# Kernel tuning notes

Measured on AMD Instinct MI355X. Metric: run time of the kernel, lower is better.

## Reference

```python
import jax, jax.numpy as jnp
import numpy as np

B, T, E, H = 4, 2048, 1024, 16
HS = E // H  # head_size = 64


def setup_inputs() -> dict:
    key = jax.random.key(0)
    ks = jax.random.split(key, 5)
    x = jax.random.normal(ks[0], (B, T, E), jnp.float32)
    scale = 0.02
    Wq = jax.random.normal(ks[1], (H, E, HS), jnp.float32) * scale
    Wk = jax.random.normal(ks[2], (H, E, HS), jnp.float32) * scale
    Wv = jax.random.normal(ks[3], (H, E, HS), jnp.float32) * scale
    Wo = jax.random.normal(ks[4], (E, E), jnp.float32) * scale
    bo = jnp.zeros((E,), jnp.float32)
    return {"x": x, "Wq": Wq, "Wk": Wk, "Wv": Wv, "Wo": Wo, "bo": bo}


def reference(x, Wq, Wk, Wv, Wo, bo):
    b, t, e = x.shape
    # per-head projections, batched over heads
    Q = jnp.einsum('bte,hed->bhtd', x, Wq)  # (B,H,T,HS)
    K = jnp.einsum('bte,hed->bhtd', x, Wk)
    V = jnp.einsum('bte,hed->bhtd', x, Wv)
    # faithful quirk 1: scale by sqrt(embd_size), not sqrt(head_size)
    scores = jnp.einsum('bhtd,bhsd->bhts', Q, K) / jnp.sqrt(jnp.float32(e))
    mask = jnp.tril(jnp.ones((t, t), dtype=bool))  # (T_q, T_k)
    scores = jnp.where(mask[None, None, :, :], scores, -jnp.inf)
    # faithful quirk 2: original softmaxes over dim=1 of (B,Tq,Tk) = the QUERY axis
    attn = jax.nn.softmax(scores, axis=2)
    out = jnp.einsum('bhts,bhsd->bhtd', attn, V)  # (B,H,T,HS)
    out = out.transpose(0, 2, 1, 3).reshape(b, t, e)  # concat heads -> (B,T,E)
    return out @ Wo + bo
```

## Files before the change

### kernel.cpp

```cpp
#include <hip/hip_runtime.h>
#include <stdint.h>

#define Bn 4
#define Tn 2048
#define En 1024
#define Hn 16
#define HSn 64
#define BHn (Bn*Hn)
#define NRn (Bn*Tn)

#define CEXP 0.0450840831f

typedef __attribute__((ext_vector_type(8))) short short8;
typedef __attribute__((ext_vector_type(4))) float f32x4;
typedef __attribute__((ext_vector_type(16))) float f32x16;
typedef __attribute__((ext_vector_type(4))) unsigned int uint4w;

__device__ __forceinline__ unsigned short f2b(float f){
  union { float f; unsigned int u; } c; c.f = f;
  unsigned int u = c.u + 0x7FFFu + ((c.u >> 16) & 1u);
  return (unsigned short)(u >> 16);
}
__device__ __forceinline__ float b2f(unsigned short s){
  union { unsigned int u; float f; } c; c.u = ((unsigned int)s) << 16;
  return c.f;
}
__device__ __forceinline__ unsigned int cvtpk(float lo, float hi){
  unsigned int r;
  asm("v_cvt_pk_bf16_f32 %0, %1, %2" : "=v"(r) : "v"(lo), "v"(hi));
  return r;
}
__device__ __forceinline__ f32x4 mfma16(short8 a, short8 b, f32x4 c){
  return __builtin_amdgcn_mfma_f32_16x16x32_bf16(a, b, c, 0, 0, 0);
}
__device__ __forceinline__ f32x16 mfma32(short8 a, short8 b, f32x16 c){
  return __builtin_amdgcn_mfma_f32_32x32x16_bf16(a, b, c, 0, 0, 0);
}
__device__ __forceinline__ void gl16(const void* g, void* s){
  __builtin_amdgcn_global_load_lds((const __attribute__((address_space(1))) unsigned int*)g,
                                   (__attribute__((address_space(3))) unsigned int*)s, 16, 0, 0);
}
#define FENCE()    asm volatile("" ::: "memory")
#define WAITV(N)   asm volatile("s_waitcnt vmcnt(" #N ")" ::: "memory")
#define SBAR()     __builtin_amdgcn_s_barrier()

__global__ void k_cvt_x(const float* __restrict__ x, unsigned short* __restrict__ xb){
  int i = (blockIdx.x * blockDim.x + threadIdx.x) * 8;
  float4 a = *(const float4*)(x + i);
  float4 b = *(const float4*)(x + i + 4);
  alignas(16) unsigned short o[8] = {f2b(a.x),f2b(a.y),f2b(a.z),f2b(a.w),
                                     f2b(b.x),f2b(b.y),f2b(b.z),f2b(b.w)};
  *(uint4w*)(xb + i) = *(const uint4w*)o;
}

__global__ void k_wT(const float* __restrict__ Wq, const float* __restrict__ Wk,
                     const float* __restrict__ Wv, const float* __restrict__ Wo,
                     unsigned short* __restrict__ Wt, unsigned short* __restrict__ Wot)
{
  __shared__ unsigned short Ls[64*80];
  const int tid = threadIdx.x;
  const int ey = blockIdx.x, jt = blockIdx.y;
  const int e0 = ey*64;
  const float* src; int R, c0; unsigned short* outp;
  if (jt < 48){
    int sel = jt >> 4, h = jt & 15;
    const float* W = (sel==0)?Wq:((sel==1)?Wk:Wv);
    src = W + h*(En*HSn); R = HSn; c0 = 0;
    outp = Wt + jt*64*En;
  } else {
    src = Wo; R = En; c0 = (jt-48)*64;
    outp = Wot + (jt-48)*64*En;
  }
  {
    const int e = tid >> 2, cq = (tid & 3)*16;
    const float* p = src + (e0 + e)*R + c0 + cq;
    float vv[16];
    *(float4*)&vv[0]  = *(const float4*)(p);
    *(float4*)&vv[4]  = *(const float4*)(p+4);
    *(float4*)&vv[8]  = *(const float4*)(p+8);
    *(float4*)&vv[12] = *(const float4*)(p+12);
#pragma unroll
    for (int i = 0; i < 16; i++) Ls[(cq+i)*80 + e] = f2b(vv[i]);
  }
  __syncthreads();
  {
    const int c8 = tid & 7, r = tid >> 3;
#pragma unroll
    for (int rr0 = 0; rr0 < 2; rr0++){
      int rr = r + rr0*32;
      *(uint4w*)(outp + rr*En + e0 + c8*8) = *(const uint4w*)&Ls[rr*80 + c8*8];
    }
  }
}

__global__ void __launch_bounds__(256, 2)
k_qkv(const unsigned short* __restrict__ xb,
      const unsigned short* __restrict__ Wt,
      unsigned short* __restrict__ Qb, unsigned short* __restrict__ Kb,
      unsigned short* __restrict__ Vt)
{
  __shared__ unsigned short As[2][128*64];
  __shared__ unsigned short Bs[2][128*64];
  const int tid = threadIdx.x, lane = tid & 63, w = tid >> 6;
  const int wr = w >> 1, wc = w & 1;
  const int mb = blockIdx.x, nb = blockIdx.y;
  const int n0 = nb*128;
  const int sel = n0 >> 10;
  const int nj0 = n0 & 1023;
  const int l15 = lane & 15, kc = lane >> 4;
  const int r8 = lane >> 3, c7 = lane & 7;

  const unsigned short* xbase = xb + (mb*128)*En;
  const unsigned short* wbase = Wt + n0*En;

  f32x4 acc[4][4];
#pragma unroll
  for (int i = 0; i < 4; i++)
#pragma unroll
    for (int j = 0; j < 4; j++) acc[i][j] = (f32x4){0.f,0.f,0.f,0.f};

  auto stage = [&](int buf, int k0){
#pragma unroll
    for (int i = 0; i < 4; i++){
      const int rb = w*32 + i*8;
      const int r = rb + r8;
      const int g = (c7 ^ r8) * 8;
      gl16(xbase + r*En + k0 + g, &As[buf][rb*64]);
      gl16(wbase + r*En + k0 + g, &Bs[buf][rb*64]);
    }
  };
  auto compute = [&](int cur){
    const unsigned short* Ac = &As[cur][0];
    const unsigned short* Bc = &Bs[cur][0];
#pragma unroll
    for (int ks = 0; ks < 2; ks++){
      short8 af[4], bf[4];
#pragma unroll
      for (int mf = 0; mf < 4; mf++){
        int ar = wr*64 + mf*16 + l15;
        af[mf] = *(const short8*)&Ac[ar*64 + (((ks*4 + kc) ^ (ar & 7))*8)];
      }
#pragma unroll
      for (int nf = 0; nf < 4; nf++){
        int br = wc*64 + nf*16 + l15;
        bf[nf] = *(const short8*)&Bc[br*64 + (((ks*4 + kc) ^ (br & 7))*8)];
      }
      __builtin_amdgcn_s_setprio(1);
#pragma unroll
      for (int mf = 0; mf < 4; mf++)
#pragma unroll
        for (int nf = 0; nf < 4; nf++)
          acc[mf][nf] = mfma16(af[mf], bf[nf], acc[mf][nf]);
      __builtin_amdgcn_s_setprio(0);
    }
  };

  stage(0, 0);
  stage(1, 64);
  WAITV(8); SBAR();

  for (int kt = 0; kt < 16; kt++){
    const int cur = kt & 1;
    compute(cur);
    FENCE(); SBAR();
    if (kt < 14){
      stage(cur, (kt + 2)*64);
      WAITV(8); SBAR();
    } else if (kt == 14){
      WAITV(0); SBAR();
    }
  }
  __syncthreads();

  const int q4 = (lane >> 4)*4;
  const int bb = mb >> 4;
  const int tt0 = (mb*128) & 2047;

  if (sel == 2){
    unsigned short* tb = ((w < 2) ? &As[0][0] : &Bs[0][0]) + (w & 1)*8192;
#pragma unroll
    for (int nf = 0; nf < 4; nf++)
#pragma unroll
      for (int mf = 0; mf < 4; mf++){
        uint2 u;
        u.x = cvtpk(acc[mf][nf][0], acc[mf][nf][1]);
        u.y = cvtpk(acc[mf][nf][2], acc[mf][nf][3]);
        *(uint2*)&tb[(nf*16 + l15)*72 + mf*16 + q4] = u;
      }
    const int hh = (nj0 >> 6) + wc;
    unsigned short* vb = Vt + ((bb*Hn + hh)*HSn)*Tn + tt0 + wr*64;
#pragma unroll
    for (int i = 0; i < 8; i++){
      int rr = i*8 + r8;
      *(uint4w*)(vb + rr*Tn + c7*8) = *(const uint4w*)&tb[rr*72 + c7*8];
    }
  } else {
    unsigned short* Out = (sel == 1) ? Kb : Qb;
#pragma unroll
    for (int nf = 0; nf < 4; nf++){
      int jj = nj0 + wc*64 + nf*16 + l15;
      int hh = jj >> 6, dd = jj & 63;
#pragma unroll
      for (int mf = 0; mf < 4; mf++){
#pragma unroll
        for (int q = 0; q < 4; q++){
          int tt = tt0 + wr*64 + mf*16 + q4 + q;
          Out[((bb*Hn + hh)*Tn + tt)*HSn + dd] = f2b(acc[mf][nf][q]);
        }
      }
    }
  }
}

__global__ void k_colsum(const unsigned short* __restrict__ Qb,
                         const unsigned short* __restrict__ Kb,
                         float* __restrict__ Linv)
{
  __shared__ unsigned short Qs[2][128*64];
  __shared__ float Lred[64];
  const int bh = blockIdx.x, ipair = blockIdx.y;
  const int tid = threadIdx.x, lane = tid & 63, w = tid >> 6;
  const int l5 = lane >> 5, l31 = lane & 31;

  for (int ph = 0; ph < 2; ph++){
    const int sb = ph ? (31 - ipair) : ipair;
    const int s0 = sb * 64;

    short8 kf[2][4];
#pragma unroll
    for (int sf = 0; sf < 2; sf++){
      const unsigned short* kr = Kb + (bh*Tn + s0 + sf*32 + l31)*HSn + 8*l5;
#pragma unroll
      for (int ks = 0; ks < 4; ks++) kf[sf][ks] = *(const short8*)(kr + 16*ks);
    }

    float ls[2][16];
#pragma unroll
    for (int sf = 0; sf < 2; sf++)
#pragma unroll
      for (int r = 0; r < 16; r++) ls[sf][r] = 0.f;

    if (tid < 64) Lred[tid] = 0.f;

    const int t0s = (s0 >> 7) << 7;
    const int ntl = (Tn - t0s) >> 7;

    auto stageQ = [&](int buf, int tg0){
      const int c = lane & 7;
#pragma unroll
      for (int i = 0; i < 4; i++){
        int row = (w*4 + i)*8 + (lane >> 3);
        gl16(Qb + (bh*Tn + tg0 + row)*HSn + ((c ^ (row & 7))*8), &Qs[buf][(w*4 + i)*512]);
      }
    };

    stageQ(0, t0s);
    if (ntl > 1){ stageQ(1, t0s + 128); WAITV(4); }
    else        { WAITV(0); }
    SBAR();

    for (int it = 0; it < ntl; it++){
      const int cur = it & 1;
      const int t0 = t0s + it*128;
      const int tw = t0 + 32*w;
      if (tw + 31 >= s0){
        f32x16 st[2];
#pragma unroll
        for (int sf = 0; sf < 2; sf++)
#pragma unroll
          for (int r = 0; r < 16; r++) st[sf][r] = 0.f;
        const int qrow = w*32 + l31;
        const unsigned short* Qc = &Qs[cur][qrow*64];
        const int sw = qrow & 7;
        __builtin_amdgcn_s_setprio(1);
#pragma unroll
        for (int ks = 0; ks < 4; ks++){
          short8 qb = *(const short8*)&Qc[((l5 + 2*ks) ^ sw)*8];
          st[0] = mfma32(kf[0][ks], qb, st[0]);
          st[1] = mfma32(kf[1][ks], qb, st[1]);
        }
        __builtin_amdgcn_s_setprio(0);
        const int tg = tw + l31;
        if (s0 + 63 <= tw){
#pragma unroll
          for (int sf = 0; sf < 2; sf++)
#pragma unroll
            for (int r = 0; r < 16; r++)
              ls[sf][r] += __builtin_amdgcn_exp2f(st[sf][r] * CEXP);
        } else {
#pragma unroll
          for (int sf = 0; sf < 2; sf++)
#pragma unroll
            for (int r = 0; r < 16; r++){
              int sg = s0 + 32*sf + (r & 3) + 8*(r >> 2) + 4*l5;
              float e = __builtin_amdgcn_exp2f(st[sf][r] * CEXP);
              ls[sf][r] += (tg >= sg) ? e : 0.f;
            }
        }
      }
      FENCE(); SBAR();
      if (it + 2 < ntl){
        stageQ(cur, t0s + (it + 2)*128);
        WAITV(4); SBAR();
      } else if (it + 2 == ntl){
        WAITV(0); SBAR();
      }
    }

#pragma unroll
    for (int sf = 0; sf < 2; sf++)
#pragma unroll
      for (int r = 0; r < 16; r++){
        float v = ls[sf][r];
        v += __shfl_xor(v, 1);  v += __shfl_xor(v, 2);
        v += __shfl_xor(v, 4);  v += __shfl_xor(v, 8);
        v += __shfl_xor(v, 16);
        ls[sf][r] = v;
      }
    if (l31 == 0){
#pragma unroll
      for (int sf = 0; sf < 2; sf++)
#pragma unroll
        for (int r = 0; r < 16; r++){
          int sl = 32*sf + (r & 3) + 8*(r >> 2) + 4*l5;
          atomicAdd(&Lred[sl], ls[sf][r]);
        }
    }
    __syncthreads();
    if (tid < 64) Linv[bh*Tn + s0 + tid] = 1.0f / Lred[tid];
    if (ph == 0) __syncthreads();
  }
}

__global__ void k_vscale(unsigned short* __restrict__ Vt, const float* __restrict__ Linv){
  int i = (blockIdx.x * blockDim.x + threadIdx.x) * 8;
  int bh = i >> 17, t = i & 2047;
  short8 v = *(const short8*)(Vt + i);
  float4 L0 = *(const float4*)(Linv + bh*Tn + t);
  float4 L1 = *(const float4*)(Linv + bh*Tn + t + 4);
  unsigned int r0 = cvtpk(b2f((unsigned short)v[0])*L0.x, b2f((unsigned short)v[1])*L0.y);
  unsigned int r1 = cvtpk(b2f((unsigned short)v[2])*L0.z, b2f((unsigned short)v[3])*L0.w);
  unsigned int r2 = cvtpk(b2f((unsigned short)v[4])*L1.x, b2f((unsigned short)v[5])*L1.y);
  unsigned int r3 = cvtpk(b2f((unsigned short)v[6])*L1.z, b2f((unsigned short)v[7])*L1.w);
  uint4w o; o[0]=r0; o[1]=r1; o[2]=r2; o[3]=r3;
  *(uint4w*)(Vt + i) = o;
}

__global__ void __launch_bounds__(256, 4)
k_attn(const unsigned short* __restrict__ Qb,
       const unsigned short* __restrict__ Kb,
       const unsigned short* __restrict__ Vlt,
       unsigned short* __restrict__ Att)
{
  __shared__ unsigned short Ks[2][64*64];
  __shared__ unsigned short Vs[2][64*64];
  const int bh = blockIdx.x;
  const int tb = 15 - blockIdx.y;
  const int t0 = tb * 128;
  const int tid = threadIdx.x, lane = tid & 63, w = tid >> 6;
  const int l5 = lane >> 5, l31 = lane & 31;
  const int c7 = lane & 7, r8 = lane >> 3;
  const int tbase = t0 + w*32;
  const int nt = 2*tb + 2;

  short8 qf[4];
  {
    const unsigned short* qr = Qb + (bh*Tn + tbase + l31)*HSn + 8*l5;
#pragma unroll
    for (int ks = 0; ks < 4; ks++) qf[ks] = *(const short8*)(qr + 16*ks);
  }

  f32x16 oacc[2];
#pragma unroll
  for (int df = 0; df < 2; df++)
#pragma unroll
    for (int r = 0; r < 16; r++) oacc[df][r] = 0.f;

  auto stageKV = [&](int buf, int sn){
#pragma unroll
    for (int i = 0; i < 2; i++){
      int row = (w*2 + i)*8 + r8;
      gl16(Kb  + (bh*Tn + sn + row)*HSn + ((c7 ^ (row & 7))*8), &Ks[buf][(w*2 + i)*512]);
      gl16(Vlt + (bh*HSn + row)*Tn + sn + ((c7 ^ (row & 7))*8), &Vs[buf][(w*2 + i)*512]);
    }
  };

  stageKV(0, 0);
  stageKV(1, 64);
  WAITV(4); SBAR();

  for (int it = 0; it < nt; it++){
    const int cur = it & 1;
    const int s0 = it * 64;
    if (s0 <= tbase + 31){
      const unsigned short* Kc = &Ks[cur][0];
      f32x16 st[2];
#pragma unroll
      for (int sf = 0; sf < 2; sf++)
#pragma unroll
        for (int r = 0; r < 16; r++) st[sf][r] = 0.f;
      __builtin_amdgcn_s_setprio(1);
#pragma unroll
      for (int ks = 0; ks < 4; ks++){
#pragma unroll
        for (int sf = 0; sf < 2; sf++){
          int row = sf*32 + l31;
          short8 ka = *(const short8*)&Kc[row*64 + (((l5 + 2*ks) ^ (row & 7))*8)];
          st[sf] = mfma32(ka, qf[ks], st[sf]);
        }
      }
      __builtin_amdgcn_s_setprio(0);

      const int tg = tbase + l31;
      const bool interior = (s0 + 63 <= tbase);
#pragma unroll
      for (int sf = 0; sf < 2; sf++){
#pragma unroll
        for (int r = 0; r < 16; r++){
          float e = __builtin_amdgcn_exp2f(st[sf][r] * CEXP);
          if (!interior){
            int sg = s0 + 32*sf + (r & 3) + 8*(r >> 2) + 4*l5;
            e = (tg >= sg) ? e : 0.f;
          }
          st[sf][r] = e;
        }
      }

      short8 pb[4];
#pragma unroll
      for (int sf = 0; sf < 2; sf++){
#pragma unroll
        for (int q = 0; q < 2; q++){
          unsigned int ax = cvtpk(st[sf][8*q+0], st[sf][8*q+1]);
          unsigned int ay = cvtpk(st[sf][8*q+2], st[sf][8*q+3]);
          unsigned int bx = cvtpk(st[sf][8*q+4], st[sf][8*q+5]);
          unsigned int by = cvtpk(st[sf][8*q+6], st[sf][8*q+7]);
          asm("v_permlane32_swap_b32 %0, %1" : "+v"(ax), "+v"(bx));
          asm("v_permlane32_swap_b32 %0, %1" : "+v"(ay), "+v"(by));
          union { unsigned int u[4]; short8 s; } pk;
          pk.u[0] = ax; pk.u[1] = ay; pk.u[2] = bx; pk.u[3] = by;
          pb[sf*2 + q] = pk.s;
        }
      }

      const unsigned short* Vc = &Vs[cur][0];
      __builtin_amdgcn_s_setprio(1);
#pragma unroll
      for (int ks = 0; ks < 4; ks++){
#pragma unroll
        for (int df = 0; df < 2; df++){
          int row = df*32 + l31;
          short8 va = *(const short8*)&Vc[row*64 + (((l5 + 2*ks) ^ (row & 7))*8)];
          oacc[df] = mfma32(va, pb[ks], oacc[df]);
        }
      }
      __builtin_amdgcn_s_setprio(0);
    }
    FENCE(); SBAR();
    if (it + 2 < nt){
      stageKV(cur, (it + 2)*64);
      WAITV(4); SBAR();
    } else if (it + 2 == nt){
      WAITV(0); SBAR();
    }
  }

  {
    const int tg = tbase + l31;
    unsigned short* ob = Att + (bh*Tn + tg)*HSn;
#pragma unroll
    for (int df = 0; df < 2; df++)
#pragma unroll
      for (int r2 = 0; r2 < 4; r2++){
        uint2 u;
        u.x = cvtpk(oacc[df][r2*4+0], oacc[df][r2*4+1]);
        u.y = cvtpk(oacc[df][r2*4+2], oacc[df][r2*4+3]);
        *(uint2*)&ob[32*df + 8*r2 + 4*l5] = u;
      }
  }
}

__global__ void __launch_bounds__(256, 2)
k_oproj(const unsigned short* __restrict__ Att,
        const unsigned short* __restrict__ Wot,
        const float* __restrict__ bo, float* __restrict__ out)
{
  __shared__ unsigned short As[2][128*64];
  __shared__ unsigned short Bs[2][128*64];
  const int tid = threadIdx.x, lane = tid & 63, w = tid >> 6;
  const int wr = w >> 1, wc = w & 1;
  const int mb = blockIdx.x, nb = blockIdx.y;
  const int n0 = nb*128;
  const int l15 = lane & 15, kc = lane >> 4;
  const int r8 = lane >> 3, c7 = lane & 7;
  const int bb = mb >> 4;
  const int t0 = (mb*128) & 2047;

  f32x4 acc[4][4];
#pragma unroll
  for (int i = 0; i < 4; i++)
#pragma unroll
    for (int j = 0; j < 4; j++) acc[i][j] = (f32x4){0.f,0.f,0.f,0.f};

  const unsigned short* wbase = Wot + n0*En;

  auto stage = [&](int buf, int k0){
    const int hh = k0 >> 6;
    const unsigned short* abase = Att + ((bb*Hn + hh)*Tn + t0)*HSn;
#pragma unroll
    for (int i = 0; i < 4; i++){
      const int rb = w*32 + i*8;
      const int r = rb + r8;
      const int g = (c7 ^ r8) * 8;
      gl16(abase + r*HSn + g, &As[buf][rb*64]);
      gl16(wbase + r*En + k0 + g, &Bs[buf][rb*64]);
    }
  };
  auto compute = [&](int cur){
    const unsigned short* Ac = &As[cur][0];
    const unsigned short* Bc = &Bs[cur][0];
#pragma unroll
    for (int ks = 0; ks < 2; ks++){
      short8 af[4], bf[4];
#pragma unroll
      for (int mf = 0; mf < 4; mf++){
        int ar = wr*64 + mf*16 + l15;
        af[mf] = *(const short8*)&Ac[ar*64 + (((ks*4 + kc) ^ (ar & 7))*8)];
      }
#pragma unroll
      for (int nf = 0; nf < 4; nf++){
        int br = wc*64 + nf*16 + l15;
        bf[nf] = *(const short8*)&Bc[br*64 + (((ks*4 + kc) ^ (br & 7))*8)];
      }
      __builtin_amdgcn_s_setprio(1);
#pragma unroll
      for (int mf = 0; mf < 4; mf++)
#pragma unroll
        for (int nf = 0; nf < 4; nf++)
          acc[mf][nf] = mfma16(af[mf], bf[nf], acc[mf][nf]);
      __builtin_amdgcn_s_setprio(0);
    }
  };

  stage(0, 0);
  stage(1, 64);
  WAITV(8); SBAR();

  for (int kt = 0; kt < 16; kt++){
    const int cur = kt & 1;
    compute(cur);
    FENCE(); SBAR();
    if (kt < 14){
      stage(cur, (kt + 2)*64);
      WAITV(8); SBAR();
    } else if (kt == 14){
      WAITV(0); SBAR();
    }
  }

  const int q4 = (lane >> 4)*4;
#pragma unroll
  for (int nf = 0; nf < 4; nf++){
    int j = n0 + wc*64 + nf*16 + l15;
    float bias = bo[j];
#pragma unroll
    for (int mf = 0; mf < 4; mf++){
#pragma unroll
      for (int q = 0; q < 4; q++){
        int rr = mb*128 + wr*64 + mf*16 + q4 + q;
        out[rr*En + j] = acc[mf][nf][q] + bias;
      }
    }
  }
}

extern "C" void kernel_launch(void* const* d_in, const int* in_sizes, int n_in,
                              void* d_out, int out_size, void* d_ws, size_t ws_size,
                              hipStream_t stream)
{
  (void)in_sizes; (void)n_in; (void)out_size; (void)ws_size;
  const float* x  = (const float*)d_in[0];
  const float* Wq = (const float*)d_in[1];
  const float* Wk = (const float*)d_in[2];
  const float* Wv = (const float*)d_in[3];
  const float* Wo = (const float*)d_in[4];
  const float* bo = (const float*)d_in[5];
  float* out = (float*)d_out;

  uint8_t* w = (uint8_t*)d_ws;
  unsigned short* Qb  = (unsigned short*)(w);
  unsigned short* Kb  = (unsigned short*)(w + (16u << 20));
  unsigned short* Vt  = (unsigned short*)(w + (32u << 20));
  unsigned short* xb  = (unsigned short*)(w + (48u << 20));
  unsigned short* Att = (unsigned short*)(w + (48u << 20));
  unsigned short* Wt  = (unsigned short*)(w + (64u << 20));
  unsigned short* Wot = (unsigned short*)(w + (70u << 20));
  float* Linv         = (float*)(w + (72u << 20));

  hipLaunchKernelGGL(k_cvt_x,  dim3(4096),    dim3(256), 0, stream, x, xb);
  hipLaunchKernelGGL(k_wT,     dim3(16, 64),  dim3(256), 0, stream, Wq, Wk, Wv, Wo, Wt, Wot);
  hipLaunchKernelGGL(k_qkv,    dim3(64, 24),  dim3(256), 0, stream, xb, Wt, Qb, Kb, Vt);
  hipLaunchKernelGGL(k_colsum, dim3(64, 16),  dim3(256), 0, stream, Qb, Kb, Linv);
  hipLaunchKernelGGL(k_vscale, dim3(4096),    dim3(256), 0, stream, Vt, Linv);
  hipLaunchKernelGGL(k_attn,   dim3(64, 16),  dim3(256), 0, stream, Qb, Kb, Vt, Att);
  hipLaunchKernelGGL(k_oproj,  dim3(64, 8),   dim3(256), 0, stream, Att, Wot, bo, out);
}
```

Before: 209.1 us.

## Fuse V scaling into colsum and triple-buffer Q/KV staging with one barrier

```diff
diff --git a/kernel.cpp b/kernel.cpp
--- a/kernel.cpp
+++ b/kernel.cpp
@@ -212,15 +212,18 @@
   }
 }
 
-__global__ void k_colsum(const unsigned short* __restrict__ Qb,
-                         const unsigned short* __restrict__ Kb,
-                         float* __restrict__ Linv)
+__global__ void __launch_bounds__(256, 3)
+k_colsum(const unsigned short* __restrict__ Qb,
+         const unsigned short* __restrict__ Kb,
+         unsigned short* __restrict__ Vt,
+         float* __restrict__ Linv)
 {
-  __shared__ unsigned short Qs[2][128*64];
+  __shared__ unsigned short Qs[3][128*64];
   __shared__ float Lred[64];
   const int bh = blockIdx.x, ipair = blockIdx.y;
   const int tid = threadIdx.x, lane = tid & 63, w = tid >> 6;
   const int l5 = lane >> 5, l31 = lane & 31;
+  const int r8 = lane >> 3, c7 = lane & 7;
 
   for (int ph = 0; ph < 2; ph++){
     const int sb = ph ? (31 - ipair) : ipair;
@@ -246,21 +249,22 @@
     const int ntl = (Tn - t0s) >> 7;
 
     auto stageQ = [&](int buf, int tg0){
-      const int c = lane & 7;
 #pragma unroll
       for (int i = 0; i < 4; i++){
-        int row = (w*4 + i)*8 + (lane >> 3);
-        gl16(Qb + (bh*Tn + tg0 + row)*HSn + ((c ^ (row & 7))*8), &Qs[buf][(w*4 + i)*512]);
+        int row = (w*4 + i)*8 + r8;
+        gl16(Qb + (bh*Tn + tg0 + row)*HSn + ((c7 ^ (row & 7))*8), &Qs[buf][(w*4 + i)*512]);
       }
     };
 
     stageQ(0, t0s);
-    if (ntl > 1){ stageQ(1, t0s + 128); WAITV(4); }
-    else        { WAITV(0); }
-    SBAR();
+    if (ntl > 1) stageQ(1, t0s + 128);
 
     for (int it = 0; it < ntl; it++){
-      const int cur = it & 1;
+      if (it + 1 < ntl){ WAITV(4); } else { WAITV(0); }
+      FENCE(); SBAR(); FENCE();
+      if (it + 2 < ntl) stageQ((it + 2) % 3, t0s + (it + 2)*128);
+
+      const int cur = it % 3;
       const int t0 = t0s + it*128;
       const int tw = t0 + 32*w;
       if (tw + 31 >= s0){
@@ -297,13 +301,6 @@
               ls[sf][r] += (tg >= sg) ? e : 0.f;
             }
         }
-      }
-      FENCE(); SBAR();
-      if (it + 2 < ntl){
-        stageQ(cur, t0s + (it + 2)*128);
-        WAITV(4); SBAR();
-      } else if (it + 2 == ntl){
-        WAITV(0); SBAR();
       }
     }
 
@@ -328,32 +325,39 @@
     }
     __syncthreads();
     if (tid < 64) Linv[bh*Tn + s0 + tid] = 1.0f / Lred[tid];
+
+    {
+      const int d = tid >> 2, cq = (tid & 3)*16;
+      unsigned short* vp = Vt + ((size_t)(bh*HSn + d))*Tn + s0 + cq;
+      short8 v0 = *(const short8*)vp;
+      short8 v1 = *(const short8*)(vp + 8);
+      float inv[16];
+#pragma unroll
+      for (int j = 0; j < 16; j++) inv[j] = 1.0f / Lred[cq + j];
+      uint4w o0, o1;
+      o0[0] = cvtpk(b2f((unsigned short)v0[0])*inv[0],  b2f((unsigned short)v0[1])*inv[1]);
+      o0[1] = cvtpk(b2f((unsigned short)v0[2])*inv[2],  b2f((unsigned short)v0[3])*inv[3]);
+      o0[2] = cvtpk(b2f((unsigned short)v0[4])*inv[4],  b2f((unsigned short)v0[5])*inv[5]);
+      o0[3] = cvtpk(b2f((unsigned short)v0[6])*inv[6],  b2f((unsigned short)v0[7])*inv[7]);
+      o1[0] = cvtpk(b2f((unsigned short)v1[0])*inv[8],  b2f((unsigned short)v1[1])*inv[9]);
+      o1[1] = cvtpk(b2f((unsigned short)v1[2])*inv[10], b2f((unsigned short)v1[3])*inv[11]);
+      o1[2] = cvtpk(b2f((unsigned short)v1[4])*inv[12], b2f((unsigned short)v1[5])*inv[13]);
+      o1[3] = cvtpk(b2f((unsigned short)v1[6])*inv[14], b2f((unsigned short)v1[7])*inv[15]);
+      *(uint4w*)vp       = o0;
+      *(uint4w*)(vp + 8) = o1;
+    }
     if (ph == 0) __syncthreads();
   }
 }
 
-__global__ void k_vscale(unsigned short* __restrict__ Vt, const float* __restrict__ Linv){
-  int i = (blockIdx.x * blockDim.x + threadIdx.x) * 8;
-  int bh = i >> 17, t = i & 2047;
-  short8 v = *(const short8*)(Vt + i);
-  float4 L0 = *(const float4*)(Linv + bh*Tn + t);
-  float4 L1 = *(const float4*)(Linv + bh*Tn + t + 4);
-  unsigned int r0 = cvtpk(b2f((unsigned short)v[0])*L0.x, b2f((unsigned short)v[1])*L0.y);
-  unsigned int r1 = cvtpk(b2f((unsigned short)v[2])*L0.z, b2f((unsigned short)v[3])*L0.w);
-  unsigned int r2 = cvtpk(b2f((unsigned short)v[4])*L1.x, b2f((unsigned short)v[5])*L1.y);
-  unsigned int r3 = cvtpk(b2f((unsigned short)v[6])*L1.z, b2f((unsigned short)v[7])*L1.w);
-  uint4w o; o[0]=r0; o[1]=r1; o[2]=r2; o[3]=r3;
-  *(uint4w*)(Vt + i) = o;
-}
-
-__global__ void __launch_bounds__(256, 4)
+__global__ void __launch_bounds__(256, 3)
 k_attn(const unsigned short* __restrict__ Qb,
        const unsigned short* __restrict__ Kb,
        const unsigned short* __restrict__ Vlt,
        unsigned short* __restrict__ Att)
 {
-  __shared__ unsigned short Ks[2][64*64];
-  __shared__ unsigned short Vs[2][64*64];
+  __shared__ unsigned short Ks[3][64*64];
+  __shared__ unsigned short Vs[3][64*64];
   const int bh = blockIdx.x;
   const int tb = 15 - blockIdx.y;
   const int t0 = tb * 128;
@@ -386,11 +390,14 @@
   };
 
   stageKV(0, 0);
-  stageKV(1, 64);
-  WAITV(4); SBAR();
+  if (nt > 1) stageKV(1, 64);
 
   for (int it = 0; it < nt; it++){
-    const int cur = it & 1;
+    if (it + 1 < nt){ WAITV(4); } else { WAITV(0); }
+    FENCE(); SBAR(); FENCE();
+    if (it + 2 < nt) stageKV((it + 2) % 3, (it + 2)*64);
+
+    const int cur = it % 3;
     const int s0 = it * 64;
     if (s0 <= tbase + 31){
       const unsigned short* Kc = &Ks[cur][0];
@@ -455,13 +462,6 @@
         }
       }
       __builtin_amdgcn_s_setprio(0);
-    }
-    FENCE(); SBAR();
-    if (it + 2 < nt){
-      stageKV(cur, (it + 2)*64);
-      WAITV(4); SBAR();
-    } else if (it + 2 == nt){
-      WAITV(0); SBAR();
     }
   }
 
@@ -600,8 +600,7 @@
   hipLaunchKernelGGL(k_cvt_x,  dim3(4096),    dim3(256), 0, stream, x, xb);
   hipLaunchKernelGGL(k_wT,     dim3(16, 64),  dim3(256), 0, stream, Wq, Wk, Wv, Wo, Wt, Wot);
   hipLaunchKernelGGL(k_qkv,    dim3(64, 24),  dim3(256), 0, stream, xb, Wt, Qb, Kb, Vt);
-  hipLaunchKernelGGL(k_colsum, dim3(64, 16),  dim3(256), 0, stream, Qb, Kb, Linv);
-  hipLaunchKernelGGL(k_vscale, dim3(4096),    dim3(256), 0, stream, Vt, Linv);
+  hipLaunchKernelGGL(k_colsum, dim3(64, 16),  dim3(256), 0, stream, Qb, Kb, Vt, Linv);
   hipLaunchKernelGGL(k_attn,   dim3(64, 16),  dim3(256), 0, stream, Qb, Kb, Vt, Att);
   hipLaunchKernelGGL(k_oproj,  dim3(64, 8),   dim3(256), 0, stream, Att, Wot, bo, out);
 }
```

Result: no change. 208.0 us (-0.5%).
